# Optimization experiments

Hardware: AMD Instinct MI355X
Metric: run time of the kernel (lower is better)

The kernel has to match this reference:

```python
import jax, jax.numpy as jnp
import numpy as np

N = 4096  # matrix is [N, N]; all entries are nonzero 'edges' (uniform(0,1) fill)


def setup_inputs() -> dict:
    key = jax.random.key(0)
    k1, k2, k3 = jax.random.split(key, 3)
    matrix = jax.random.uniform(k1, (N, N), dtype=jnp.float32)
    drop_param = jax.random.normal(k2, (1,), dtype=jnp.float32)
    gamma = jax.random.normal(k3, (1,), dtype=jnp.float32)
    return {"matrix": matrix, "drop_param": drop_param, "gamma": gamma,
            "drop_ratio_pct": 20}


def reference(matrix, drop_param, gamma, drop_ratio_pct):
    # Flatten: every nonzero entry is an edge. With uniform fill all N*N entries
    # are edges, so num_edges is static and k is a trace-time Python int.
    v = matrix.reshape(-1)                       # [E] edge values
    num_edges = v.shape[0]
    k = (num_edges * drop_ratio_pct) // 100      # int(num_edges * drop_ratio)

    # drop_prob = sigmoid(drop_param*(1 - v) - gamma*v)  (per-edge weight)
    logits = drop_param[0] * (1.0 - v) - gamma[0] * v
    logp = jax.nn.log_sigmoid(logits)            # log of unnormalized weight

    # Weighted sampling without replacement (Efraimidis-Spirakis / Gumbel top-k):
    # taking top-k of log(p_i) + Gumbel_i samples k indices w/o replacement with
    # probability proportional to p_i (normalization is a shift, top-k invariant).
    u = jax.random.uniform(jax.random.key(42), (num_edges,), dtype=jnp.float32,
                           minval=1e-7, maxval=1.0 - 1e-7)
    gumbel = -jnp.log(-jnp.log(u))
    keys = jnp.where(v != 0, logp + gumbel, -jnp.inf)  # only real edges eligible
    _, drop_idx = jax.lax.top_k(keys, k)         # [k] sampled edge indices

    # Vectorized scatter of zeros (replaces the Python for-loop in the original)
    dropped = v.at[drop_idx].set(0.0)
    return dropped.reshape(matrix.shape)
```

## Files before the change

kernel.cpp:

```cpp
#include <hip/hip_runtime.h>
#include <hip/hip_bf16.h>
#include <stdint.h>


#define NBINS 8192
#define NBINS_SHIFT 19
#define NBS 256
#define NBSTREAM 1024
#define STREAM_T 512
#define NB2 512
#define LIST_CAP 2097152u
#define MINI_CAP 16384u
#define LBUF_CAP 2048
#define TIES_TILE 4096
#define SLACK 2
#define MARGIN 2.0e-4f

__device__ __forceinline__ unsigned tf_bits(unsigned i) {
  const unsigned ks0 = 0u;
  const unsigned ks1 = 42u;
  const unsigned ks2 = 0x1BD11BDAu ^ 0u ^ 42u;
  unsigned x0 = 0u + ks0;
  unsigned x1 = i + ks1;
#define TF_R(rot) { x0 += x1; \
  x1 = __builtin_amdgcn_alignbit(x1, x1, 32u - (rot)); x1 ^= x0; }
  TF_R(13) TF_R(15) TF_R(26) TF_R(6)
  x0 += ks1; x1 += ks2 + 1u;
  TF_R(17) TF_R(29) TF_R(16) TF_R(24)
  x0 += ks2; x1 += ks0 + 2u;
  TF_R(13) TF_R(15) TF_R(26) TF_R(6)
  x0 += ks0; x1 += ks1 + 3u;
  TF_R(17) TF_R(29) TF_R(16) TF_R(24)
  x0 += ks1; x1 += ks2 + 4u;
  TF_R(13) TF_R(15) TF_R(26) TF_R(6)
  x0 += ks2; x1 += ks0 + 5u;
#undef TF_R
  return x0 ^ x1;
}

__device__ __forceinline__ float uniform_from_bits(unsigned bits) {
  unsigned fb = (bits >> 9) | 0x3f800000u;
  float f = __uint_as_float(fb) - 1.0f;
  const float minv = 1e-7f;
  const float maxv = __uint_as_float(0x3F7FFFFEu);
  float r = __fsub_rn(maxv, minv);
  float u = __fadd_rn(__fmul_rn(f, r), minv);
  return fmaxf(minv, u);
}

__device__ __forceinline__ float xla_expf(float input) {
  const float exp_hi = 88.3762626647950f;
  const float exp_lo = -88.3762626647949f;
  float x = fminf(fmaxf(input, exp_lo), exp_hi);
  float fx = floorf(__fadd_rn(__fmul_rn(x, 1.44269504088896341f), 0.5f));
  float tmp = __fmul_rn(0.693359375f, fx);
  float z = __fmul_rn(-2.12194440e-4f, fx);
  x = __fsub_rn(x, tmp);
  x = __fsub_rn(x, z);
  z = __fmul_rn(x, x);
  float y = __fadd_rn(__fmul_rn(x, 1.9875691500e-4f), 1.3981999507e-3f);
  y = __fadd_rn(__fmul_rn(y, x), 8.3334519073e-3f);
  y = __fadd_rn(__fmul_rn(y, x), 4.1665795894e-2f);
  y = __fadd_rn(__fmul_rn(y, x), 1.6666665459e-1f);
  y = __fadd_rn(__fmul_rn(y, x), 5.0000001201e-1f);
  y = __fadd_rn(__fmul_rn(y, z), x);
  y = __fadd_rn(1.0f, y);
  int n = (int)fx;
  float p2n = __int_as_float((n + 0x7f) << 23);
  return fmaxf(__fmul_rn(y, p2n), input);
}

__device__ __forceinline__ float xla_logf(float input) {
  float t0 = fmaxf(input, __uint_as_float(0x00800000u));
  unsigned ib = __float_as_uint(t0);
  int emm0 = (int)(ib >> 23) - 0x7f;
  float e = __fadd_rn(1.0f, (float)emm0);
  float m = __uint_as_float((ib & 0x807fffffu) | 0x3f000000u);
  bool mask = m < 0.707106781186547524f;
  float t1 = mask ? m : 0.0f;
  m = __fsub_rn(m, 1.0f);
  e = __fsub_rn(e, mask ? 1.0f : 0.0f);
  m = __fadd_rn(m, t1);
  float x2 = __fmul_rn(m, m);
  float x3 = __fmul_rn(x2, m);
  float y  = __fadd_rn(__fmul_rn(m, 7.0376836292e-2f), -1.1514610310e-1f);
  float y1 = __fadd_rn(__fmul_rn(m, -1.2420140846e-1f), 1.4249322787e-1f);
  float y2 = __fadd_rn(__fmul_rn(m, 2.0000714765e-1f), -2.4999993993e-1f);
  y  = __fadd_rn(__fmul_rn(y, m), 1.1676998740e-1f);
  y1 = __fadd_rn(__fmul_rn(y1, m), -1.6668057665e-1f);
  y2 = __fadd_rn(__fmul_rn(y2, m), 3.3333331174e-1f);
  y = __fadd_rn(__fmul_rn(y, x3), y1);
  y = __fadd_rn(__fmul_rn(y, x3), y2);
  y = __fmul_rn(y, x3);
  y = __fadd_rn(y, __fmul_rn(-2.12194440e-4f, e));
  y = __fsub_rn(y, __fmul_rn(0.5f, x2));
  m = __fadd_rn(m, y);
  m = __fadd_rn(m, __fmul_rn(0.693359375f, e));
  return m;
}

__device__ __forceinline__ float xla_log1pf(float x) {
  float for_large = xla_logf(__fadd_rn(x, 1.0f));
  float for_small = __fmul_rn(__fadd_rn(__fmul_rn(-0.5f, x), 1.0f), x);
  return (fabsf(x) < 1e-4f) ? for_small : for_large;
}

__device__ __forceinline__ unsigned encode_f(float f) {
  unsigned b = __float_as_uint(f);
  return (b & 0x80000000u) ? ~b : (b | 0x80000000u);
}
__device__ __forceinline__ float decode_f(unsigned c) {
  unsigned b = (c & 0x80000000u) ? (c ^ 0x80000000u) : ~c;
  return __uint_as_float(b);
}

__device__ __forceinline__ unsigned compute_ou(unsigned i, float v, float dp, float g) {
  if (v == 0.0f) return 0u;
  unsigned bits = tf_bits(i);
  float u = uniform_from_bits(bits);
  float lg = xla_logf(u);
  float gum = -xla_logf(-lg);
  float t = __fsub_rn(1.0f, v);
  float lx = __fsub_rn(__fmul_rn(dp, t), __fmul_rn(g, v));
  float ex = xla_expf(-fabsf(lx));
  float l1p = xla_log1pf(ex);
  float lp = -(__fadd_rn(fmaxf(-lx, 0.0f), l1p));
  float key = __fadd_rn(lp, gum);
  return encode_f(key);
}

__device__ __forceinline__ float approx_key(unsigned i, float v, float dp, float g) {
  if (v == 0.0f) return -INFINITY;
  unsigned bits = tf_bits(i);
  float u = uniform_from_bits(bits);
  float lg = __logf(u);
  float gum = -__logf(-lg);
  float t = __fsub_rn(1.0f, v);
  float lx = __fsub_rn(__fmul_rn(dp, t), __fmul_rn(g, v));
  float ex = __expf(-fabsf(lx));
  float for_small = __fmul_rn(__fadd_rn(__fmul_rn(-0.5f, ex), 1.0f), ex);
  float l1p = (fabsf(ex) < 1e-4f) ? for_small : __logf(__fadd_rn(ex, 1.0f));
  float lp = -(__fadd_rn(fmaxf(-lx, 0.0f), l1p));
  return __fadd_rn(lp, gum);
}

__device__ __forceinline__ void set_band(unsigned* state, int B, int w) {
  int plo = B - w; if (plo < 32) plo = 32;
  int phi = B + w;
  unsigned blo_c = (unsigned)plo << NBINS_SHIFT;
  float blo_v = decode_f(blo_c);
  float bhi_v; unsigned bhi_c;
  if (phi >= NBINS - 1) { bhi_v = INFINITY; bhi_c = encode_f(INFINITY); }
  else { bhi_c = (unsigned)(phi + 1) << NBINS_SHIFT; bhi_v = decode_f(bhi_c); }
  float clo_v = blo_v + MARGIN;
  float chi_v = bhi_v - MARGIN;
  state[2] = blo_c; state[3] = bhi_c;
  state[16] = __float_as_uint(blo_v);
  state[17] = __float_as_uint(bhi_v);
  state[18] = __float_as_uint(clo_v);
  state[19] = __float_as_uint(chi_v);
  float Cb = __expf(-blo_v);
  float Cl = __expf(-clo_v);
  float Ch = (chi_v == INFINITY) ? 0.0f : __expf(-chi_v);
  float Cd = (bhi_v == INFINITY) ? 0.0f : __expf(-bhi_v);
  state[23] = __float_as_uint(Cb);
  state[24] = __float_as_uint(Cd);
  state[25] = __float_as_uint(Cl);
  state[26] = __float_as_uint(Ch);
  state[22] = (isfinite(Cb) && isfinite(Cl)) ? 0u : 1u;
  unsigned span = bhi_c - blo_c;
  unsigned sh = 0;
  while ((span >> sh) >= 4096u) ++sh;
  state[12] = sh;
}

__global__ __launch_bounds__(256) void sample_hist_kernel(
    const float* __restrict__ v, const float* __restrict__ dpp,
    const float* __restrict__ gp, unsigned* __restrict__ hist_s,
    int nvec, int chunk, int spb) {
  __shared__ unsigned h[NBINS];
  for (int j = threadIdx.x; j < NBINS; j += 256) h[j] = 0;
  __syncthreads();
  float dp = dpp[0], g = gp[0];
  int t = threadIdx.x;
  if (t < spb) {
    int iv = blockIdx.x * chunk + t;
    if (iv < nvec) {
      float4 vv = reinterpret_cast<const float4*>(v)[iv];
      unsigned base = (unsigned)iv << 2;
      atomicAdd(&h[encode_f(approx_key(base + 0u, vv.x, dp, g)) >> NBINS_SHIFT], 1u);
      atomicAdd(&h[encode_f(approx_key(base + 1u, vv.y, dp, g)) >> NBINS_SHIFT], 1u);
      atomicAdd(&h[encode_f(approx_key(base + 2u, vv.z, dp, g)) >> NBINS_SHIFT], 1u);
      atomicAdd(&h[encode_f(approx_key(base + 3u, vv.w, dp, g)) >> NBINS_SHIFT], 1u);
    }
  }
  __syncthreads();
  for (int j = threadIdx.x; j < NBINS; j += 256)
    if (h[j]) atomicAdd(&hist_s[j], h[j]);
}

__global__ __launch_bounds__(1024) void find_sample_kernel(
    const unsigned* __restrict__ hist_s, unsigned* __restrict__ state,
    const int* __restrict__ pct_p, long long Etot, long long SN) {
  __shared__ unsigned s[1024];
  __shared__ int bs_sh;
  int t = threadIdx.x;
  if (t == 0) bs_sh = NBINS / 2;
  unsigned hh[8];
  unsigned tot = 0;
  #pragma unroll
  for (int j = 0; j < 8; ++j) { hh[j] = hist_s[t * 8 + j]; tot += hh[j]; }
  s[t] = tot;
  __syncthreads();
  for (int off = 1; off < 1024; off <<= 1) {
    unsigned add = (t + off < 1024) ? s[t + off] : 0u;
    __syncthreads();
    s[t] += add;
    __syncthreads();
  }
  long long k = (Etot * (long long)pct_p[0]) / 100;
  long long ks = (Etot > 0) ? (k * SN) / Etot : 0;
  if (ks < 1) ks = 1;
  long long above_next = (t < 1023) ? (long long)s[t + 1] : 0;
  if (above_next < ks && ks <= above_next + (long long)tot) {
    long long above = above_next;
    for (int b = 7; b >= 0; --b) {
      if (above < ks && ks <= above + (long long)hh[b]) { bs_sh = t * 8 + b; break; }
      above += (long long)hh[b];
    }
  }
  __syncthreads();
  if (t == 0) {
    state[6] = (unsigned)k;
    state[0] = (unsigned)bs_sh;
    if (k == 0) {
      state[15] = 0u; state[22] = 0u;
      state[2] = 0xFFFFFFFFu; state[3] = 0xFFFFFFFFu; state[12] = 0u;
      state[16] = state[17] = state[18] = state[19] = __float_as_uint(INFINITY);
      state[23] = state[24] = state[25] = state[26] = 0u;
    } else {
      set_band(state, bs_sh, SLACK);
    }
  }
}

__global__ __launch_bounds__(STREAM_T) void stream_kernel(
    const float* __restrict__ v, const float* __restrict__ dpp,
    const float* __restrict__ gp, float* __restrict__ out,
    unsigned* __restrict__ state, uint2* __restrict__ list, int E, int mode) {
  if (mode == 1 && state[15] == 0u) return;
  __shared__ uint2 lbuf[LBUF_CAP];
  __shared__ unsigned lcnt, lbase, s_a, s_hi, s_lo;
  if (threadIdx.x == 0) { lcnt = 0; s_a = 0; s_hi = 0; s_lo = 0; }
  __syncthreads();
  float dp = dpp[0], g = gp[0];
  int nvec = E >> 2;
  int stride = gridDim.x * STREAM_T;
  unsigned a_c = 0, hi_c = 0, lo_c = 0;

  if (state[22] == 0u) {
    float Cb = __uint_as_float(state[23]);
    float Cd = __uint_as_float(state[24]);
    float Cl = __uint_as_float(state[25]);
    float Ch = __uint_as_float(state[26]);
    float A = __fadd_rn(dp, g);
    for (int iv = blockIdx.x * STREAM_T + threadIdx.x; iv < nvec; iv += stride) {
      float4 vv = reinterpret_cast<const float4*>(v)[iv];
      unsigned base = (unsigned)iv << 2;
      float vals[4] = {vv.x, vv.y, vv.z, vv.w};
      float q[4];
      #pragma unroll
      for (int j = 0; j < 4; ++j) {
        unsigned bits = tf_bits(base + (unsigned)j);
        float u = uniform_from_bits(bits);
        float w = -__logf(u);
        float lx = __fmaf_rn(-A, vals[j], dp);
        float ex = __expf(-lx);
        float qq = __fmaf_rn(w, ex, w);
        q[j] = (vals[j] == 0.0f) ? INFINITY : qq;
      }
      float res[4];
      #pragma unroll
      for (int j = 0; j < 4; ++j) {
        bool drop = q[j] < Cd;
        a_c  += drop ? 1u : 0u;
        hi_c += (q[j] <= Ch) ? 1u : 0u;
        lo_c += (q[j] <= Cl) ? 1u : 0u;
        res[j] = drop ? 0.0f : vals[j];
        if (!drop && q[j] <= Cb) {
          unsigned p = atomicAdd(&lcnt, 1u);
          uint2 ent = make_uint2(base + (unsigned)j, __float_as_uint(vals[j]));
          if (p < LBUF_CAP) lbuf[p] = ent;
          else {
            unsigned qg = atomicAdd(&state[4], 1u);
            if (qg < LIST_CAP) list[qg] = ent;
          }
        }
      }
      float4 oo; oo.x = res[0]; oo.y = res[1]; oo.z = res[2]; oo.w = res[3];
      reinterpret_cast<float4*>(out)[iv] = oo;
    }
  } else {
    float blo_v = __uint_as_float(state[16]);
    float bhi_v = __uint_as_float(state[17]);
    float clo_v = __uint_as_float(state[18]);
    float chi_v = __uint_as_float(state[19]);
    for (int iv = blockIdx.x * STREAM_T + threadIdx.x; iv < nvec; iv += stride) {
      float4 vv = reinterpret_cast<const float4*>(v)[iv];
      unsigned base = (unsigned)iv << 2;
      float vals[4] = {vv.x, vv.y, vv.z, vv.w};
      float kk[4];
      #pragma unroll
      for (int j = 0; j < 4; ++j) kk[j] = approx_key(base + (unsigned)j, vals[j], dp, g);
      float res[4];
      #pragma unroll
      for (int j = 0; j < 4; ++j) {
        bool drop = kk[j] > bhi_v;
        a_c  += drop ? 1u : 0u;
        hi_c += (kk[j] >= chi_v) ? 1u : 0u;
        lo_c += (kk[j] >= clo_v) ? 1u : 0u;
        res[j] = drop ? 0.0f : vals[j];
        if (!drop && kk[j] >= blo_v) {
          unsigned p = atomicAdd(&lcnt, 1u);
          uint2 ent = make_uint2(base + (unsigned)j, __float_as_uint(vals[j]));
          if (p < LBUF_CAP) lbuf[p] = ent;
          else {
            unsigned qg = atomicAdd(&state[4], 1u);
            if (qg < LIST_CAP) list[qg] = ent;
          }
        }
      }
      float4 oo; oo.x = res[0]; oo.y = res[1]; oo.z = res[2]; oo.w = res[3];
      reinterpret_cast<float4*>(out)[iv] = oo;
    }
  }
  if (blockIdx.x == 0) {
    float blo_v = __uint_as_float(state[16]);
    float bhi_v = __uint_as_float(state[17]);
    float clo_v = __uint_as_float(state[18]);
    float chi_v = __uint_as_float(state[19]);
    for (int i = (nvec << 2) + threadIdx.x; i < E; i += STREAM_T) {
      float val = v[i];
      float key = approx_key((unsigned)i, val, dp, g);
      bool drop = key > bhi_v;
      a_c  += drop ? 1u : 0u;
      hi_c += (key >= chi_v) ? 1u : 0u;
      lo_c += (key >= clo_v) ? 1u : 0u;
      out[i] = drop ? 0.0f : val;
      if (!drop && key >= blo_v) {
        unsigned p = atomicAdd(&lcnt, 1u);
        uint2 ent = make_uint2((unsigned)i, __float_as_uint(val));
        if (p < LBUF_CAP) lbuf[p] = ent;
        else {
          unsigned qg = atomicAdd(&state[4], 1u);
          if (qg < LIST_CAP) list[qg] = ent;
        }
      }
    }
  }
  #pragma unroll
  for (int off = 32; off > 0; off >>= 1) {
    a_c  += __shfl_xor(a_c, off);
    hi_c += __shfl_xor(hi_c, off);
    lo_c += __shfl_xor(lo_c, off);
  }
  if ((threadIdx.x & 63) == 0) {
    if (a_c)  atomicAdd(&s_a, a_c);
    if (hi_c) atomicAdd(&s_hi, hi_c);
    if (lo_c) atomicAdd(&s_lo, lo_c);
  }
  __syncthreads();
  if (threadIdx.x == 0) {
    lbase = atomicAdd(&state[4], min(lcnt, (unsigned)LBUF_CAP));
    if (s_a)  atomicAdd(&state[5], s_a);
    if (s_hi) atomicAdd(&state[20], s_hi);
    if (s_lo) atomicAdd(&state[21], s_lo);
  }
  __syncthreads();
  unsigned n = min(lcnt, (unsigned)LBUF_CAP);
  for (unsigned j = threadIdx.x; j < n; j += STREAM_T) {
    unsigned q = lbase + j;
    if (q < LIST_CAP) list[q] = lbuf[j];
  }
}

__global__ __launch_bounds__(64) void find_verify_kernel(
    unsigned* __restrict__ state) {
  if (threadIdx.x != 0) return;
  unsigned k = state[6];
  if (k == 0u) { state[15] = 0u; return; }
  unsigned hi = state[20], lo = state[21], M = state[4];
  bool cond_hi = hi < k;
  bool cond_lo = lo >= k;
  bool cond_M = M <= LIST_CAP;
  if (cond_hi && cond_lo && cond_M) { state[15] = 0u; return; }
  state[15] = 1u;
  int B = (int)state[0];
  int w = SLACK;
  if (!cond_hi)      B += 2 * SLACK - 1;
  else if (!cond_lo) B -= 2 * SLACK - 1;
  else               w = 1;
  state[0] = (unsigned)B;
  set_band(state, B, w);
  state[4] = 0u; state[5] = 0u; state[20] = 0u; state[21] = 0u;
}

__device__ __forceinline__ unsigned band_bin(unsigned ec, unsigned blo,
                                             unsigned span, unsigned sh) {
  if (ec <= blo) return 0u;
  unsigned d = ec - blo;
  if (d > span) d = span;
  return d >> sh;
}

__global__ __launch_bounds__(256) void exact_eval_kernel(
    const float* __restrict__ dpp, const float* __restrict__ gp,
    const uint2* __restrict__ list, unsigned* __restrict__ elist,
    const unsigned* __restrict__ state, unsigned* __restrict__ blockhist2) {
  __shared__ unsigned h[4096];
  for (int j = threadIdx.x; j < 4096; j += 256) h[j] = 0;
  __syncthreads();
  unsigned M = min(state[4], LIST_CAP);
  unsigned blo = state[2], span = state[3] - state[2], sh = state[12];
  float dp = dpp[0], g = gp[0];
  for (unsigned e = blockIdx.x * 256 + threadIdx.x; e < M; e += gridDim.x * 256) {
    uint2 le = list[e];
    unsigned ec = compute_ou(le.x, __uint_as_float(le.y), dp, g);
    elist[e] = ec;
    atomicAdd(&h[band_bin(ec, blo, span, sh)], 1u);
  }
  __syncthreads();
  unsigned* row = blockhist2 + (size_t)blockIdx.x * 4096;
  for (int j = threadIdx.x; j < 4096; j += 256) row[j] = h[j];
}

__global__ __launch_bounds__(256) void reduce_hist2_kernel(
    const unsigned* __restrict__ blockhist2, unsigned* __restrict__ hist2) {
  int j = blockIdx.x * 256 + threadIdx.x;
  unsigned s = 0;
  for (int b = 0; b < NB2; ++b) s += blockhist2[(size_t)b * 4096 + j];
  hist2[j] = s;
}

__global__ __launch_bounds__(1024) void find_band_kernel(
    const unsigned* __restrict__ hist2, unsigned* __restrict__ state) {
  __shared__ unsigned s[1024];
  int t = threadIdx.x;
  unsigned hh[4];
  unsigned tot = 0;
  #pragma unroll
  for (int j = 0; j < 4; ++j) { hh[j] = hist2[t * 4 + j]; tot += hh[j]; }
  s[t] = tot;
  __syncthreads();
  for (int off = 1; off < 1024; off <<= 1) {
    unsigned add = (t + off < 1024) ? s[t + off] : 0u;
    __syncthreads();
    s[t] += add;
    __syncthreads();
  }
  unsigned kp = state[6] - state[5];
  if (kp == 0u || kp > s[0]) {
    if (t == 0) { state[7] = 0xFFFFFFFFu; state[8] = 0u; }
    return;
  }
  unsigned above_next = (t < 1023) ? s[t + 1] : 0u;
  if (above_next < kp && kp <= s[t]) {
    unsigned above = above_next;
    for (int b = 3; b >= 0; --b) {
      if (above < kp && kp <= above + hh[b]) {
        state[7] = (unsigned)(t * 4 + b);
        state[8] = kp - above;
        break;
      }
      above += hh[b];
    }
  }
}

__global__ __launch_bounds__(256) void band_drop_kernel(
    const uint2* __restrict__ list, const unsigned* __restrict__ elist,
    unsigned* __restrict__ state, float* __restrict__ out,
    uint2* __restrict__ mini) {
  unsigned M = min(state[4], LIST_CAP);
  unsigned Eb = state[7];
  unsigned blo = state[2], span = state[3] - state[2], sh = state[12];
  for (unsigned e = blockIdx.x * 256 + threadIdx.x; e < M; e += gridDim.x * 256) {
    unsigned ec = elist[e];
    unsigned bin = band_bin(ec, blo, span, sh);
    if (bin > Eb) out[list[e].x] = 0.0f;
    else if (bin == Eb) {
      unsigned q = atomicAdd(&state[11], 1u);
      if (q < MINI_CAP) mini[q] = make_uint2(ec, list[e].x);
    }
  }
}

__global__ __launch_bounds__(1024) void mini_ties_kernel(
    const uint2* __restrict__ mini, const unsigned* __restrict__ state,
    float* __restrict__ out) {
  __shared__ uint2 tile[TIES_TILE];
  unsigned m = min(state[11], MINI_CAP);
  unsigned r = state[8];
  if (r == 0u || m == 0u) return;
  int tid = threadIdx.x;
  for (unsigned e0 = 0; e0 < m; e0 += blockDim.x) {
    unsigned e = e0 + tid;
    bool valid = e < m;
    unsigned my_ec = 0, my_idx = 0;
    if (valid) { uint2 me = mini[e]; my_ec = me.x; my_idx = me.y; }
    unsigned rank = 0;
    for (unsigned t0 = 0; t0 < m; t0 += TIES_TILE) {
      unsigned tn = min((unsigned)TIES_TILE, m - t0);
      __syncthreads();
      for (unsigned j = tid; j < tn; j += blockDim.x) tile[j] = mini[t0 + j];
      __syncthreads();
      if (valid) {
        for (unsigned j = 0; j < tn; ++j) {
          uint2 o = tile[j];
          rank += (o.x > my_ec || (o.x == my_ec && o.y < my_idx)) ? 1u : 0u;
        }
      }
    }
    if (valid && rank < r) out[my_idx] = 0.0f;
  }
}

extern "C" void kernel_launch(void* const* d_in, const int* in_sizes, int n_in,
                              void* d_out, int out_size, void* d_ws, size_t ws_size,
                              hipStream_t stream) {
  const float* v  = (const float*)d_in[0];
  const float* dp = (const float*)d_in[1];
  const float* g  = (const float*)d_in[2];
  const int* pct  = (const int*)d_in[3];
  float* out = (float*)d_out;
  int E = in_sizes[0];

  uint8_t* ws = (uint8_t*)d_ws;
  const size_t STATE_OFF = 0;
  const size_t HISTS_OFF = 4 * 1024;
  const size_t HIST2_OFF = 64 * 1024;
  const size_t MINI_OFF  = 128 * 1024;
  const size_t BH2_OFF   = (size_t)1 << 20;
  const size_t LIST_OFF  = (size_t)9 << 20;
  const size_t ELIST_OFF = (size_t)25 << 20;
  const size_t NEED = ELIST_OFF + (size_t)LIST_CAP * 4;

  if (ws_size < NEED) {
    hipMemcpyAsync(out, v, (size_t)E * 4, hipMemcpyDeviceToDevice, stream);
    return;
  }

  unsigned* state  = (unsigned*)(ws + STATE_OFF);
  unsigned* hist_s = (unsigned*)(ws + HISTS_OFF);
  unsigned* hist2  = (unsigned*)(ws + HIST2_OFF);
  uint2*    mini   = (uint2*)(ws + MINI_OFF);
  unsigned* bh2    = (unsigned*)(ws + BH2_OFF);
  uint2*    list   = (uint2*)(ws + LIST_OFF);
  unsigned* elist  = (unsigned*)(ws + ELIST_OFF);

  int nvec = E >> 2;
  int chunk = (nvec + NBS - 1) / NBS;
  int spb = chunk < 256 ? chunk : 256;
  long long SN = (long long)NBS * (long long)spb * 4;

  hipMemsetAsync(ws, 0, 40 * 1024, stream);

  sample_hist_kernel<<<NBS, 256, 0, stream>>>(v, dp, g, hist_s, nvec, chunk, spb);
  find_sample_kernel<<<1, 1024, 0, stream>>>(hist_s, state, pct, (long long)E, SN);
  stream_kernel<<<NBSTREAM, STREAM_T, 0, stream>>>(v, dp, g, out, state, list, E, 0);
  find_verify_kernel<<<1, 64, 0, stream>>>(state);
  stream_kernel<<<NBSTREAM, STREAM_T, 0, stream>>>(v, dp, g, out, state, list, E, 1);
  exact_eval_kernel<<<NB2, 256, 0, stream>>>(dp, g, list, elist, state, bh2);
  reduce_hist2_kernel<<<16, 256, 0, stream>>>(bh2, hist2);
  find_band_kernel<<<1, 1024, 0, stream>>>(hist2, state);
  band_drop_kernel<<<256, 256, 0, stream>>>(list, elist, state, out, mini);
  mini_ties_kernel<<<1, 1024, 0, stream>>>(mini, state, out);
}
```

Before: 127.4 us.

## Fuse single-block finalize kernels into producers via last-block-done atomics

Merges each single-block follow-up kernel (find_sample, find_verify, reduce/find_band, mini_ties) into its producer kernel using a last-arriving-block pattern built on atomic counters and threadfences. This cuts the pipeline from ten launches to five. Per-block histograms now go straight to global atomics, so the separate reduction buffer is gone. The stream kernel's inner math moves to exp2/log2 builtins with LOG2E-scaled thresholds, and block counts for sampling, eval and band-drop are reduced. In exchange, the finalize steps run on one block at the tail of a larger kernel, and correctness depends on the fence and atomic-load ordering.

```diff
diff --git a/kernel.cpp b/kernel.cpp
--- a/kernel.cpp
+++ b/kernel.cpp
@@ -5,16 +5,22 @@
 
 #define NBINS 8192
 #define NBINS_SHIFT 19
-#define NBS 256
+#define NBS 64
 #define NBSTREAM 1024
 #define STREAM_T 512
-#define NB2 512
+#define NB2 128
+#define NB3 64
 #define LIST_CAP 2097152u
 #define MINI_CAP 16384u
 #define LBUF_CAP 2048
-#define TIES_TILE 4096
+#define TIES_TILE 2048
 #define SLACK 2
 #define MARGIN 2.0e-4f
+#define LOG2E 1.44269504088896340736f
+
+__device__ __forceinline__ unsigned aload(const unsigned* p) {
+  return __hip_atomic_load(p, __ATOMIC_RELAXED, __HIP_MEMORY_SCOPE_AGENT);
+}
 
 __device__ __forceinline__ unsigned tf_bits(unsigned i) {
   const unsigned ks0 = 0u;
@@ -159,10 +165,10 @@
   state[17] = __float_as_uint(bhi_v);
   state[18] = __float_as_uint(clo_v);
   state[19] = __float_as_uint(chi_v);
-  float Cb = __expf(-blo_v);
-  float Cl = __expf(-clo_v);
-  float Ch = (chi_v == INFINITY) ? 0.0f : __expf(-chi_v);
-  float Cd = (bhi_v == INFINITY) ? 0.0f : __expf(-bhi_v);
+  float Cb = __expf(-blo_v) * LOG2E;
+  float Cl = __expf(-clo_v) * LOG2E;
+  float Ch = (chi_v == INFINITY) ? 0.0f : __expf(-chi_v) * LOG2E;
+  float Cd = (bhi_v == INFINITY) ? 0.0f : __expf(-bhi_v) * LOG2E;
   state[23] = __float_as_uint(Cb);
   state[24] = __float_as_uint(Cd);
   state[25] = __float_as_uint(Cl);
@@ -174,15 +180,19 @@
   state[12] = sh;
 }
 
-__global__ __launch_bounds__(256) void sample_hist_kernel(
+__global__ __launch_bounds__(1024) void sample_hist_kernel(
     const float* __restrict__ v, const float* __restrict__ dpp,
     const float* __restrict__ gp, unsigned* __restrict__ hist_s,
-    int nvec, int chunk, int spb) {
+    unsigned* __restrict__ state, const int* __restrict__ pct_p,
+    long long Etot, int nvec, int chunk, int spb, long long SN) {
   __shared__ unsigned h[NBINS];
-  for (int j = threadIdx.x; j < NBINS; j += 256) h[j] = 0;
+  __shared__ unsigned s[1024];
+  __shared__ int bs_sh;
+  __shared__ unsigned rank_s;
+  int t = threadIdx.x;
+  for (int j = t; j < NBINS; j += 1024) h[j] = 0;
   __syncthreads();
   float dp = dpp[0], g = gp[0];
-  int t = threadIdx.x;
   if (t < spb) {
     int iv = blockIdx.x * chunk + t;
     if (iv < nvec) {
@@ -195,21 +205,19 @@
     }
   }
   __syncthreads();
-  for (int j = threadIdx.x; j < NBINS; j += 256)
+  for (int j = t; j < NBINS; j += 1024)
     if (h[j]) atomicAdd(&hist_s[j], h[j]);
-}
-
-__global__ __launch_bounds__(1024) void find_sample_kernel(
-    const unsigned* __restrict__ hist_s, unsigned* __restrict__ state,
-    const int* __restrict__ pct_p, long long Etot, long long SN) {
-  __shared__ unsigned s[1024];
-  __shared__ int bs_sh;
-  int t = threadIdx.x;
+  __threadfence();
+  __syncthreads();
+  if (t == 0) rank_s = atomicAdd(&state[30], 1u);
+  __syncthreads();
+  if (rank_s != (unsigned)(gridDim.x - 1)) return;
+  __threadfence();
   if (t == 0) bs_sh = NBINS / 2;
   unsigned hh[8];
   unsigned tot = 0;
   #pragma unroll
-  for (int j = 0; j < 8; ++j) { hh[j] = hist_s[t * 8 + j]; tot += hh[j]; }
+  for (int j = 0; j < 8; ++j) { hh[j] = aload(&hist_s[t * 8 + j]); tot += hh[j]; }
   s[t] = tot;
   __syncthreads();
   for (int off = 1; off < 1024; off <<= 1) {
@@ -250,7 +258,7 @@
     unsigned* __restrict__ state, uint2* __restrict__ list, int E, int mode) {
   if (mode == 1 && state[15] == 0u) return;
   __shared__ uint2 lbuf[LBUF_CAP];
-  __shared__ unsigned lcnt, lbase, s_a, s_hi, s_lo;
+  __shared__ unsigned lcnt, lbase, s_a, s_hi, s_lo, rank_s;
   if (threadIdx.x == 0) { lcnt = 0; s_a = 0; s_hi = 0; s_lo = 0; }
   __syncthreads();
   float dp = dpp[0], g = gp[0];
@@ -263,7 +271,8 @@
     float Cd = __uint_as_float(state[24]);
     float Cl = __uint_as_float(state[25]);
     float Ch = __uint_as_float(state[26]);
-    float A = __fadd_rn(dp, g);
+    float A2 = __fmul_rn(__fadd_rn(dp, g), LOG2E);
+    float dp2 = __fmul_rn(dp, LOG2E);
     for (int iv = blockIdx.x * STREAM_T + threadIdx.x; iv < nvec; iv += stride) {
       float4 vv = reinterpret_cast<const float4*>(v)[iv];
       unsigned base = (unsigned)iv << 2;
@@ -273,10 +282,9 @@
       for (int j = 0; j < 4; ++j) {
         unsigned bits = tf_bits(base + (unsigned)j);
         float u = uniform_from_bits(bits);
-        float w = -__logf(u);
-        float lx = __fmaf_rn(-A, vals[j], dp);
-        float ex = __expf(-lx);
-        float qq = __fmaf_rn(w, ex, w);
+        float w2 = -__builtin_amdgcn_logf(u);
+        float e2 = __builtin_amdgcn_exp2f(__fmaf_rn(A2, vals[j], -dp2));
+        float qq = __fmaf_rn(w2, e2, w2);
         q[j] = (vals[j] == 0.0f) ? INFINITY : qq;
       }
       float res[4];
@@ -382,27 +390,33 @@
     unsigned q = lbase + j;
     if (q < LIST_CAP) list[q] = lbuf[j];
   }
-}
-
-__global__ __launch_bounds__(64) void find_verify_kernel(
-    unsigned* __restrict__ state) {
-  if (threadIdx.x != 0) return;
-  unsigned k = state[6];
-  if (k == 0u) { state[15] = 0u; return; }
-  unsigned hi = state[20], lo = state[21], M = state[4];
-  bool cond_hi = hi < k;
-  bool cond_lo = lo >= k;
-  bool cond_M = M <= LIST_CAP;
-  if (cond_hi && cond_lo && cond_M) { state[15] = 0u; return; }
-  state[15] = 1u;
-  int B = (int)state[0];
-  int w = SLACK;
-  if (!cond_hi)      B += 2 * SLACK - 1;
-  else if (!cond_lo) B -= 2 * SLACK - 1;
-  else               w = 1;
-  state[0] = (unsigned)B;
-  set_band(state, B, w);
-  state[4] = 0u; state[5] = 0u; state[20] = 0u; state[21] = 0u;
+  if (mode != 0) return;
+  __threadfence();
+  __syncthreads();
+  if (threadIdx.x == 0) rank_s = atomicAdd(&state[31], 1u);
+  __syncthreads();
+  if (rank_s != (unsigned)(gridDim.x - 1)) return;
+  __threadfence();
+  if (threadIdx.x == 0) {
+    unsigned k = aload(&state[6]);
+    if (k == 0u) { state[15] = 0u; return; }
+    unsigned hi = aload(&state[20]);
+    unsigned lo = aload(&state[21]);
+    unsigned M  = aload(&state[4]);
+    bool cond_hi = hi < k;
+    bool cond_lo = lo >= k;
+    bool cond_M = M <= LIST_CAP;
+    if (cond_hi && cond_lo && cond_M) { state[15] = 0u; return; }
+    state[15] = 1u;
+    int B = (int)state[0];
+    int w = SLACK;
+    if (!cond_hi)      B += 2 * SLACK - 1;
+    else if (!cond_lo) B -= 2 * SLACK - 1;
+    else               w = 1;
+    state[0] = (unsigned)B;
+    set_band(state, B, w);
+    state[4] = 0u; state[5] = 0u; state[20] = 0u; state[21] = 0u;
+  }
 }
 
 __device__ __forceinline__ unsigned band_bin(unsigned ec, unsigned blo,
@@ -416,59 +430,54 @@
 __global__ __launch_bounds__(256) void exact_eval_kernel(
     const float* __restrict__ dpp, const float* __restrict__ gp,
     const uint2* __restrict__ list, unsigned* __restrict__ elist,
-    const unsigned* __restrict__ state, unsigned* __restrict__ blockhist2) {
+    unsigned* __restrict__ state, unsigned* __restrict__ hist2) {
   __shared__ unsigned h[4096];
-  for (int j = threadIdx.x; j < 4096; j += 256) h[j] = 0;
+  __shared__ unsigned sb[256];
+  __shared__ unsigned rank_s;
+  int t = threadIdx.x;
+  for (int j = t; j < 4096; j += 256) h[j] = 0;
   __syncthreads();
   unsigned M = min(state[4], LIST_CAP);
   unsigned blo = state[2], span = state[3] - state[2], sh = state[12];
   float dp = dpp[0], g = gp[0];
-  for (unsigned e = blockIdx.x * 256 + threadIdx.x; e < M; e += gridDim.x * 256) {
+  for (unsigned e = blockIdx.x * 256 + t; e < M; e += gridDim.x * 256) {
     uint2 le = list[e];
     unsigned ec = compute_ou(le.x, __uint_as_float(le.y), dp, g);
     elist[e] = ec;
     atomicAdd(&h[band_bin(ec, blo, span, sh)], 1u);
   }
   __syncthreads();
-  unsigned* row = blockhist2 + (size_t)blockIdx.x * 4096;
-  for (int j = threadIdx.x; j < 4096; j += 256) row[j] = h[j];
-}
-
-__global__ __launch_bounds__(256) void reduce_hist2_kernel(
-    const unsigned* __restrict__ blockhist2, unsigned* __restrict__ hist2) {
-  int j = blockIdx.x * 256 + threadIdx.x;
-  unsigned s = 0;
-  for (int b = 0; b < NB2; ++b) s += blockhist2[(size_t)b * 4096 + j];
-  hist2[j] = s;
-}
-
-__global__ __launch_bounds__(1024) void find_band_kernel(
-    const unsigned* __restrict__ hist2, unsigned* __restrict__ state) {
-  __shared__ unsigned s[1024];
-  int t = threadIdx.x;
-  unsigned hh[4];
+  for (int j = t; j < 4096; j += 256)
+    if (h[j]) atomicAdd(&hist2[j], h[j]);
+  __threadfence();
+  __syncthreads();
+  if (t == 0) rank_s = atomicAdd(&state[32], 1u);
+  __syncthreads();
+  if (rank_s != (unsigned)(gridDim.x - 1)) return;
+  __threadfence();
+  unsigned hh[16];
   unsigned tot = 0;
   #pragma unroll
-  for (int j = 0; j < 4; ++j) { hh[j] = hist2[t * 4 + j]; tot += hh[j]; }
-  s[t] = tot;
-  __syncthreads();
-  for (int off = 1; off < 1024; off <<= 1) {
-    unsigned add = (t + off < 1024) ? s[t + off] : 0u;
+  for (int j = 0; j < 16; ++j) { hh[j] = aload(&hist2[t * 16 + j]); tot += hh[j]; }
+  sb[t] = tot;
+  __syncthreads();
+  for (int off = 1; off < 256; off <<= 1) {
+    unsigned add = (t + off < 256) ? sb[t + off] : 0u;
     __syncthreads();
-    s[t] += add;
+    sb[t] += add;
     __syncthreads();
   }
-  unsigned kp = state[6] - state[5];
-  if (kp == 0u || kp > s[0]) {
+  unsigned kp = aload(&state[6]) - aload(&state[5]);
+  if (kp == 0u || kp > sb[0]) {
     if (t == 0) { state[7] = 0xFFFFFFFFu; state[8] = 0u; }
     return;
   }
-  unsigned above_next = (t < 1023) ? s[t + 1] : 0u;
-  if (above_next < kp && kp <= s[t]) {
+  unsigned above_next = (t < 255) ? sb[t + 1] : 0u;
+  if (above_next < kp && kp <= sb[t]) {
     unsigned above = above_next;
-    for (int b = 3; b >= 0; --b) {
+    for (int b = 15; b >= 0; --b) {
       if (above < kp && kp <= above + hh[b]) {
-        state[7] = (unsigned)(t * 4 + b);
+        state[7] = (unsigned)(t * 16 + b);
         state[8] = kp - above;
         break;
       }
@@ -481,10 +490,13 @@
     const uint2* __restrict__ list, const unsigned* __restrict__ elist,
     unsigned* __restrict__ state, float* __restrict__ out,
     uint2* __restrict__ mini) {
+  __shared__ uint2 tile[TIES_TILE];
+  __shared__ unsigned rank_s;
+  int t = threadIdx.x;
   unsigned M = min(state[4], LIST_CAP);
   unsigned Eb = state[7];
   unsigned blo = state[2], span = state[3] - state[2], sh = state[12];
-  for (unsigned e = blockIdx.x * 256 + threadIdx.x; e < M; e += gridDim.x * 256) {
+  for (unsigned e = blockIdx.x * 256 + t; e < M; e += gridDim.x * 256) {
     unsigned ec = elist[e];
     unsigned bin = band_bin(ec, blo, span, sh);
     if (bin > Eb) out[list[e].x] = 0.0f;
@@ -493,26 +505,31 @@
       if (q < MINI_CAP) mini[q] = make_uint2(ec, list[e].x);
     }
   }
-}
-
-__global__ __launch_bounds__(1024) void mini_ties_kernel(
-    const uint2* __restrict__ mini, const unsigned* __restrict__ state,
-    float* __restrict__ out) {
-  __shared__ uint2 tile[TIES_TILE];
-  unsigned m = min(state[11], MINI_CAP);
+  __threadfence();
+  __syncthreads();
+  if (t == 0) rank_s = atomicAdd(&state[33], 1u);
+  __syncthreads();
+  if (rank_s != (unsigned)(gridDim.x - 1)) return;
+  __threadfence();
+  unsigned m = min(aload(&state[11]), MINI_CAP);
   unsigned r = state[8];
   if (r == 0u || m == 0u) return;
-  int tid = threadIdx.x;
-  for (unsigned e0 = 0; e0 < m; e0 += blockDim.x) {
-    unsigned e = e0 + tid;
+  for (unsigned e0 = 0; e0 < m; e0 += 256) {
+    unsigned e = e0 + t;
     bool valid = e < m;
     unsigned my_ec = 0, my_idx = 0;
-    if (valid) { uint2 me = mini[e]; my_ec = me.x; my_idx = me.y; }
+    if (valid) {
+      const unsigned* mp = (const unsigned*)&mini[e];
+      my_ec = aload(mp); my_idx = aload(mp + 1);
+    }
     unsigned rank = 0;
     for (unsigned t0 = 0; t0 < m; t0 += TIES_TILE) {
       unsigned tn = min((unsigned)TIES_TILE, m - t0);
       __syncthreads();
-      for (unsigned j = tid; j < tn; j += blockDim.x) tile[j] = mini[t0 + j];
+      for (unsigned j = t; j < tn; j += 256) {
+        const unsigned* mp = (const unsigned*)&mini[t0 + j];
+        tile[j] = make_uint2(aload(mp), aload(mp + 1));
+      }
       __syncthreads();
       if (valid) {
         for (unsigned j = 0; j < tn; ++j) {
@@ -538,15 +555,14 @@
   uint8_t* ws = (uint8_t*)d_ws;
   const size_t STATE_OFF = 0;
   const size_t HISTS_OFF = 4 * 1024;
-  const size_t HIST2_OFF = 64 * 1024;
-  const size_t MINI_OFF  = 128 * 1024;
-  const size_t BH2_OFF   = (size_t)1 << 20;
-  const size_t LIST_OFF  = (size_t)9 << 20;
-  const size_t ELIST_OFF = (size_t)25 << 20;
+  const size_t HIST2_OFF = 36 * 1024;
+  const size_t MINI_OFF  = 64 * 1024;
+  const size_t LIST_OFF  = (size_t)1 << 20;
+  const size_t ELIST_OFF = (size_t)17 << 20;
   const size_t NEED = ELIST_OFF + (size_t)LIST_CAP * 4;
 
   if (ws_size < NEED) {
-    hipMemcpyAsync(out, v, (size_t)E * 4, hipMemcpyDeviceToDevice, stream);
+    (void)hipMemcpyAsync(out, v, (size_t)E * 4, hipMemcpyDeviceToDevice, stream);
     return;
   }
 
@@ -554,25 +570,20 @@
   unsigned* hist_s = (unsigned*)(ws + HISTS_OFF);
   unsigned* hist2  = (unsigned*)(ws + HIST2_OFF);
   uint2*    mini   = (uint2*)(ws + MINI_OFF);
-  unsigned* bh2    = (unsigned*)(ws + BH2_OFF);
   uint2*    list   = (uint2*)(ws + LIST_OFF);
   unsigned* elist  = (unsigned*)(ws + ELIST_OFF);
 
   int nvec = E >> 2;
   int chunk = (nvec + NBS - 1) / NBS;
-  int spb = chunk < 256 ? chunk : 256;
+  int spb = chunk < 1024 ? chunk : 1024;
   long long SN = (long long)NBS * (long long)spb * 4;
 
-  hipMemsetAsync(ws, 0, 40 * 1024, stream);
-
-  sample_hist_kernel<<<NBS, 256, 0, stream>>>(v, dp, g, hist_s, nvec, chunk, spb);
-  find_sample_kernel<<<1, 1024, 0, stream>>>(hist_s, state, pct, (long long)E, SN);
+  (void)hipMemsetAsync(ws, 0, 52 * 1024, stream);
+
+  sample_hist_kernel<<<NBS, 1024, 0, stream>>>(v, dp, g, hist_s, state, pct,
+                                               (long long)E, nvec, chunk, spb, SN);
   stream_kernel<<<NBSTREAM, STREAM_T, 0, stream>>>(v, dp, g, out, state, list, E, 0);
-  find_verify_kernel<<<1, 64, 0, stream>>>(state);
   stream_kernel<<<NBSTREAM, STREAM_T, 0, stream>>>(v, dp, g, out, state, list, E, 1);
-  exact_eval_kernel<<<NB2, 256, 0, stream>>>(dp, g, list, elist, state, bh2);
-  reduce_hist2_kernel<<<16, 256, 0, stream>>>(bh2, hist2);
-  find_band_kernel<<<1, 1024, 0, stream>>>(hist2, state);
-  band_drop_kernel<<<256, 256, 0, stream>>>(list, elist, state, out, mini);
-  mini_ties_kernel<<<1, 1024, 0, stream>>>(mini, state, out);
-}
+  exact_eval_kernel<<<NB2, 256, 0, stream>>>(dp, g, list, elist, state, hist2);
+  band_drop_kernel<<<NB3, 256, 0, stream>>>(list, elist, state, out, mini);
+}
```

New measurement: 345.7 us. 2.71x slower.
